# Kernel optimization log

Hardware: AMD Instinct MI355X
Metric: run time of the kernel (lower is better)

Reference implementation:

```python
import jax, jax.numpy as jnp
import numpy as np
import math

B, C, L = 64, 16, 4096
EMB, DEPTH, NEXP = 256, 2, 4
SHAPE, STRIDE = 8, 4
NPATCH = (L - SHAPE) // STRIDE + 1  # 1023
SPARSE = 0.5
NF = 32

def gelu(x):
    return jax.nn.gelu(x, approximate=False)

def conv1d(x, w, stride=1, pad=0):
    return jax.lax.conv_general_dilated(x, w, (stride,), [(pad, pad)],
                                        dimension_numbers=('NCH', 'OIH', 'NCH'))

def rmsnorm(x, g):
    # F.normalize(x, dim=-1) * gamma * sqrt(D)
    n = jnp.sqrt(jnp.sum(x * x, axis=-1, keepdims=True))
    return x / jnp.maximum(n, 1e-12) * g * (x.shape[-1] ** 0.5)

def setup_inputs():
    ks = jax.random.split(jax.random.key(0), 16)
    r = lambda i, s: jax.random.normal(ks[i], s, jnp.float32) * 0.02
    return dict(
        x=jax.random.normal(ks[0], (B, C, L), jnp.float32),
        epoch=100, warm_up=50,
        emb_w=r(1, (EMB, C, SHAPE)), emb_b=jnp.zeros((EMB,), jnp.float32),
        pos_embed=r(2, (1, NPATCH, EMB)),
        attn_w1=r(3, (EMB, 8)), attn_b1=jnp.zeros((8,), jnp.float32),
        attn_w2=r(4, (8, 1)), attn_b2=jnp.zeros((1,), jnp.float32),
        gate_w=r(5, (EMB, NEXP)), gate_b=jnp.zeros((NEXP,), jnp.float32),
        ex_w1=r(6, (NEXP, EMB, EMB)), ex_b1=jnp.zeros((NEXP, EMB), jnp.float32),
        ex_w2=r(7, (NEXP, EMB, EMB)), ex_b2=jnp.zeros((NEXP, EMB), jnp.float32),
        moe_gamma=jnp.ones((EMB,), jnp.float32),
        norm1_g=jnp.ones((DEPTH, EMB), jnp.float32),
        norm2_g=jnp.ones((DEPTH, EMB), jnp.float32),
        bott_w=r(8, (DEPTH, NF, EMB, 1)),
        conv_w39=r(9, (DEPTH, NF, NF, 39)),
        conv_w19=r(10, (DEPTH, NF, NF, 19)),
        conv_w9=r(11, (DEPTH, NF, NF, 9)),
        mp_w=r(12, (DEPTH, NF, EMB, 1)),
        bn_g=jnp.ones((DEPTH, 4 * NF), jnp.float32),
        bn_b=jnp.zeros((DEPTH, 4 * NF), jnp.float32),
        proj_w=r(13, (DEPTH, 4 * NF, EMB)),
        proj_b=jnp.zeros((DEPTH, EMB), jnp.float32),
        head_w=r(14, (EMB, 1)), head_b=jnp.zeros((1,), jnp.float32),
    )

def _forward(x, epoch, warm_up, emb_w, emb_b, pos_embed, attn_w1, attn_b1,
             attn_w2, attn_b2, gate_w, gate_b, ex_w1, ex_b1, ex_w2, ex_b2,
             moe_gamma, norm1_g, norm2_g, bott_w, conv_w39, conv_w19, conv_w9,
             mp_w, bn_g, bn_b, proj_w, proj_b, head_w, head_b):
    def attn(h):  # (B,N,D) -> (B,N,1) sigmoid importance scores
        return jax.nn.sigmoid(jnp.tanh(h @ attn_w1 + attn_b1) @ attn_w2 + attn_b2)

    def moe(h):  # top-1 routed MoE; compute all experts densely, select via one-hot
        Bm, Nm, D = h.shape
        hf = h.reshape(-1, D)  # (T, D)
        logits = jax.nn.softmax(hf @ gate_w + gate_b, axis=-1)  # (T, E)
        top_idx = jnp.argmax(logits, axis=-1)
        top_val = jnp.max(logits, axis=-1, keepdims=True)
        mid = gelu(jnp.einsum('td,edh->eth', hf, ex_w1) + ex_b1[:, None, :])
        ye = jnp.einsum('eth,ehd->etd', mid, ex_w2) + ex_b2[:, None, :]
        sel = jax.nn.one_hot(top_idx, NEXP, dtype=h.dtype)  # (T, E)
        out = jnp.einsum('etd,te->td', ye, sel)
        y = rmsnorm((hf + out * top_val).reshape(Bm, Nm, D), moe_gamma)
        imp = logits.sum(0)
        load = jnp.var(imp, ddof=1) / (imp.mean() ** 2 + 1e-10)
        return gelu(y), load

    def inception(xc, i):  # xc: (B, D, T) -> (B, 4*NF, T)
        xb = conv1d(xc, bott_w[i])  # bottleneck 1x1 -> NF channels
        mp = jax.lax.reduce_window(xc, -jnp.inf, jax.lax.max, (1, 1, 3),
                                   (1, 1, 1), [(0, 0), (0, 0), (1, 1)])
        out = jnp.concatenate([conv1d(xb, conv_w39[i], pad=19),
                               conv1d(xb, conv_w19[i], pad=9),
                               conv1d(xb, conv_w9[i], pad=4),
                               conv1d(mp, mp_w[i])], axis=1)
        # BatchNorm1d eval mode: running mean 0 / var 1, affine gamma/beta
        out = out * (bn_g[i] / np.float32(np.sqrt(1.0 + 1e-5)))[None, :, None] \
              + bn_b[i][None, :, None]
        return gelu(out)

    def incep_branch(h, i):  # (B,N,D) -> (B,N,D)
        io = inception(jnp.transpose(h, (0, 2, 1)), i)
        return jnp.transpose(io, (0, 2, 1)) @ proj_w[i] + proj_b[i]

    h = conv1d(x, emb_w, stride=STRIDE) + emb_b[None, :, None]  # (B, EMB, N)
    h = jnp.transpose(h, (0, 2, 1)) + pos_embed  # N == NPATCH -> no interp
    # pos_drop is identity at inference

    schedule = np.linspace(0.0, SPARSE, DEPTH)
    total_loss = jnp.zeros((), h.dtype)
    end_scores = None
    for i in range(DEPTH):
        ratio = 1.0 if epoch < warm_up else 1.0 - float(schedule[i])
        is_last = (i == DEPTH - 1)
        N = h.shape[1]
        x_n = rmsnorm(h, norm1_g[i])
        scores = attn(x_n)  # (B, N, 1)
        if ratio < 1.0 and N > 2:
            left_k = max(math.ceil(ratio * N), 1)
            xs = x_n * scores
            idx = jnp.sort(jax.lax.top_k(scores[..., 0], left_k)[1], axis=1)
            left_x = jnp.take_along_axis(xs, idx[:, :, None], axis=1)
            # sum of non-topk tokens == total sum minus topk sum
            extra = xs.sum(1, keepdims=True) - left_x.sum(1, keepdims=True)
            h = jnp.concatenate([left_x, extra], axis=1)  # (B, left_k+1, D)
            x_n2 = rmsnorm(h, norm2_g[i])
            moe_out, loss = moe(x_n2)
            h = h + moe_out + incep_branch(x_n2, i)
            total_loss = total_loss + loss
        else:
            h = x_n * scores
            h = h + incep_branch(rmsnorm(h, norm2_g[i]), i)
        if is_last:
            end_scores = attn(h)  # dropout identity; scores on pre-gelu x
        h = gelu(h)
    logits = h @ head_w + head_b  # (B, N', 1)
    cls = (logits * end_scores).mean(axis=1)  # (B, 1)
    return cls[..., 0], total_loss

def reference(x, epoch, warm_up, emb_w, emb_b, pos_embed, attn_w1, attn_b1,
              attn_w2, attn_b2, gate_w, gate_b, ex_w1, ex_b1, ex_w2, ex_b2,
              moe_gamma, norm1_g, norm2_g, bott_w, conv_w39, conv_w19, conv_w9,
              mp_w, bn_g, bn_b, proj_w, proj_b, head_w, head_b):
    return _forward(x, epoch, warm_up, emb_w, emb_b, pos_embed, attn_w1,
                    attn_b1, attn_w2, attn_b2, gate_w, gate_b, ex_w1, ex_b1,
                    ex_w2, ex_b2, moe_gamma, norm1_g, norm2_g, bott_w,
                    conv_w39, conv_w19, conv_w9, mp_w, bn_g, bn_b, proj_w,
                    proj_b, head_w, head_b)
```

## Files before the change

### kernel.cpp

```cpp
#include <hip/hip_runtime.h>
#include <math.h>

#define BB 64
#define EMB 256
#define N0 1023
#define N1 513
#define NTOK0 (BB * N0)
#define NTOK1 (BB * N1)
#define GCH 16

typedef __attribute__((ext_vector_type(8))) short short8;
typedef __attribute__((ext_vector_type(4))) float f32x4;

__device__ __forceinline__ float gelu_f(float x) {
    return 0.5f * x * (1.0f + erff(x * 0.7071067811865476f));
}

__device__ __forceinline__ float4 gelu4(float4 v) {
    return make_float4(gelu_f(v.x), gelu_f(v.y), gelu_f(v.z), gelu_f(v.w));
}

__device__ __forceinline__ float wave_reduce(float v) {
#pragma unroll
    for (int o = 32; o > 0; o >>= 1) v += __shfl_down(v, o, 64);
    return v;
}

__device__ __forceinline__ unsigned short f2bf(float f) {
    unsigned int u = __float_as_uint(f);
    u = (u + 0x7FFFu + ((u >> 16) & 1u)) >> 16;
    return (unsigned short)u;
}
__device__ __forceinline__ float bf2f(unsigned short h) {
    return __uint_as_float(((unsigned int)h) << 16);
}
__device__ __forceinline__ float4 bf4_to_f4(ushort4 h) {
    return make_float4(bf2f(h.x), bf2f(h.y), bf2f(h.z), bf2f(h.w));
}

__global__ void transpose_fused(const float* __restrict__ bott, float* __restrict__ bwt0,
                                float* __restrict__ bwt1,
                                const float* __restrict__ mpw, float* __restrict__ mwt0,
                                float* __restrict__ mwt1,
                                float* __restrict__ imp, int* __restrict__ counts) {
    int idx = blockIdx.x * 256 + threadIdx.x;
    if (blockIdx.x == 0 && threadIdx.x >= 252) {
        int i = threadIdx.x - 252;
        imp[i] = 0.0f; counts[i] = 0;
    }
    const float* src; float* dst; int base;
    if (idx < 8192)        { src = bott;         dst = bwt0;  base = 0; }
    else if (idx < 16384)  { src = bott + 8192;  dst = bwt1;  base = 8192; }
    else if (idx < 24576)  { src = mpw;          dst = mwt0;  base = 16384; }
    else if (idx < 32768)  { src = mpw + 8192;   dst = mwt1;  base = 24576; }
    else return;
    int local = idx - base;
    int o = local / 256, ik = local % 256;
    dst[ik * 32 + o] = src[local];
}

__global__ void convert_bf16(const float* __restrict__ ew1, const float* __restrict__ ew2,
                             const float* __restrict__ pjw,
                             const float* __restrict__ cw39, const float* __restrict__ cw19,
                             const float* __restrict__ cw9, const float* __restrict__ embw,
                             unsigned short* __restrict__ w1t, unsigned short* __restrict__ w2t,
                             unsigned short* __restrict__ pjwb,
                             unsigned short* __restrict__ cwh, unsigned short* __restrict__ cwl,
                             unsigned short* __restrict__ ewh, unsigned short* __restrict__ ewl) {
    int idx = blockIdx.x * 256 + threadIdx.x;
    if (idx < 262144) {
        int e = idx >> 16, r = idx & 65535, n = r >> 8, k = r & 255;
        w1t[idx] = f2bf(ew1[(e << 16) + (k << 8) + n]);
    } else if (idx < 524288) {
        int j = idx - 262144;
        int e = j >> 16, r = j & 65535, n = r >> 8, k = r & 255;
        w2t[j] = f2bf(ew2[(e << 16) + (k << 8) + n]);
    } else if (idx < 589824) {
        pjwb[idx - 524288] = f2bf(pjw[idx - 524288]);
    } else if (idx < 727040) {
        int j = idx - 589824;
        int d = j / 68608, r = j % 68608;
        const float* src; int KT, rr;
        if (r < 39936)      { src = cw39; KT = 39; rr = r; }
        else if (r < 59392) { src = cw19; KT = 19; rr = r - 39936; }
        else                { src = cw9;  KT = 9;  rr = r - 59392; }
        int KK = KT * 32;
        int fo = rr / KK, jj = rr % KK, k = jj >> 5, fi = jj & 31;
        float w = src[(((d * 32 + fo) * 32) + fi) * KT + k];
        unsigned short h = f2bf(w);
        cwh[j] = h;
        cwl[j] = f2bf(w - bf2f(h));
    } else if (idx < 759808) {
        int j = idx - 727040;
        float w = embw[j];
        unsigned short h = f2bf(w);
        ewh[j] = h;
        ewl[j] = f2bf(w - bf2f(h));
    }
}

__global__ __launch_bounds__(256, 2)
void embed_mfma(const float* __restrict__ x, const unsigned short* __restrict__ ewh,
                const unsigned short* __restrict__ ewl, const float* __restrict__ emb_b,
                const float* __restrict__ pos, float* __restrict__ A) {
    int b = blockIdx.y;
    int n0 = blockIdx.x * 64;
    __shared__ __align__(16) unsigned short tokh[64 * 128];
    __shared__ __align__(16) unsigned short tokl[64 * 128];
    int tid = threadIdx.x;
#pragma unroll
    for (int it = 0; it < 4; it++) {
        int idx = tid + it * 256;
        int m = idx & 63, c = idx >> 6;
        int tok = n0 + m;
        float v[8] = {0.f, 0.f, 0.f, 0.f, 0.f, 0.f, 0.f, 0.f};
        if (tok < N0) {
            const float* p = x + ((size_t)b * 16 + c) * 4096 + 4 * tok;
            float4 a = *(const float4*)p;
            float4 bq = *(const float4*)(p + 4);
            v[0] = a.x; v[1] = a.y; v[2] = a.z; v[3] = a.w;
            v[4] = bq.x; v[5] = bq.y; v[6] = bq.z; v[7] = bq.w;
        }
        short8 hv, lv;
#pragma unroll
        for (int j = 0; j < 8; j++) {
            unsigned short hh = f2bf(v[j]);
            hv[j] = (short)hh;
            lv[j] = (short)f2bf(v[j] - bf2f(hh));
        }
        int si = (m << 7) + ((c << 3) ^ ((m & 7) << 3));
        *(short8*)(&tokh[si]) = hv;
        *(short8*)(&tokl[si]) = lv;
    }
    __syncthreads();

    int lane = tid & 63, wid = tid >> 6;
    int nb = wid << 6;
    int arow = lane & 15;
    int kgrp = (lane >> 4) << 3;
    int rb = (lane >> 4) << 2;

    f32x4 acc[4][4];
#pragma unroll
    for (int mt = 0; mt < 4; mt++)
#pragma unroll
        for (int nt = 0; nt < 4; nt++) acc[mt][nt] = f32x4{0.f, 0.f, 0.f, 0.f};

    for (int ks = 0; ks < 4; ks++) {
        int kk = (ks << 5) + kgrp;
        short8 ah[4], al[4], bh[4], bl[4];
#pragma unroll
        for (int mt = 0; mt < 4; mt++) {
            int m = (mt << 4) + arow;
            int si = (m << 7) + (kk ^ ((m & 7) << 3));
            ah[mt] = *(const short8*)(&tokh[si]);
            al[mt] = *(const short8*)(&tokl[si]);
        }
#pragma unroll
        for (int nt = 0; nt < 4; nt++) {
            int n = nb + (nt << 4) + arow;
            bh[nt] = *(const short8*)(&ewh[(n << 7) + kk]);
            bl[nt] = *(const short8*)(&ewl[(n << 7) + kk]);
        }
#pragma unroll
        for (int mt = 0; mt < 4; mt++) {
#pragma unroll
            for (int nt = 0; nt < 4; nt++) {
                acc[mt][nt] = __builtin_amdgcn_mfma_f32_16x16x32_bf16(ah[mt], bh[nt], acc[mt][nt], 0, 0, 0);
                acc[mt][nt] = __builtin_amdgcn_mfma_f32_16x16x32_bf16(al[mt], bh[nt], acc[mt][nt], 0, 0, 0);
                acc[mt][nt] = __builtin_amdgcn_mfma_f32_16x16x32_bf16(ah[mt], bl[nt], acc[mt][nt], 0, 0, 0);
            }
        }
    }

    float eb[4];
#pragma unroll
    for (int nt = 0; nt < 4; nt++) eb[nt] = emb_b[nb + (nt << 4) + arow];
#pragma unroll
    for (int mt = 0; mt < 4; mt++) {
#pragma unroll
        for (int nt = 0; nt < 4; nt++) {
            int n = nb + (nt << 4) + arow;
#pragma unroll
            for (int r = 0; r < 4; r++) {
                int m = (mt << 4) + rb + r;
                int tok = n0 + m;
                if (tok < N0)
                    A[((size_t)b * N0 + tok) * 256 + n] =
                        acc[mt][nt][r] + eb[nt] + pos[(size_t)tok * 256 + n];
            }
        }
    }
}

__global__ void norm_attn_kernel(const float* __restrict__ in, float* __restrict__ outv,
                                 float* __restrict__ score_out, const float* __restrict__ g,
                                 const float* __restrict__ w1, const float* __restrict__ b1,
                                 const float* __restrict__ w2, const float* __restrict__ b2,
                                 int scale_out, int pregelu,
                                 float* __restrict__ outv2, const float* __restrict__ g2,
                                 int T) {
    int wid = threadIdx.x >> 6, lane = threadIdx.x & 63;
    int t = blockIdx.x * 4 + wid;
    if (t >= T) return;
    float4 v = ((const float4*)(in + (size_t)t * 256))[lane];
    if (pregelu) v = gelu4(v);
    float4 xn = v;
    if (g != nullptr) {
        float ss = v.x * v.x + v.y * v.y + v.z * v.z + v.w * v.w;
        ss = wave_reduce(ss);
        ss = __shfl(ss, 0, 64);
        float inv = 16.0f / fmaxf(sqrtf(ss), 1e-12f);
        float4 g4 = ((const float4*)g)[lane];
        xn.x = v.x * inv * g4.x; xn.y = v.y * inv * g4.y;
        xn.z = v.z * inv * g4.z; xn.w = v.w * inv * g4.w;
    }
    float p[8];
#pragma unroll
    for (int j = 0; j < 8; j++) p[j] = 0.0f;
    const float xv[4] = {xn.x, xn.y, xn.z, xn.w};
#pragma unroll
    for (int c = 0; c < 4; c++) {
        const float4* wr = (const float4*)(w1 + (4 * lane + c) * 8);
        float4 wa = wr[0], wb = wr[1];
        float xx = xv[c];
        p[0] += xx * wa.x; p[1] += xx * wa.y; p[2] += xx * wa.z; p[3] += xx * wa.w;
        p[4] += xx * wb.x; p[5] += xx * wb.y; p[6] += xx * wb.z; p[7] += xx * wb.w;
    }
#pragma unroll
    for (int j = 0; j < 8; j++) p[j] = wave_reduce(p[j]);
    float sc = 0.0f;
    if (lane == 0) {
        float z = b2[0];
#pragma unroll
        for (int j = 0; j < 8; j++) z += tanhf(p[j] + b1[j]) * w2[j];
        sc = 1.0f / (1.0f + expf(-z));
        if (score_out) score_out[t] = sc;
    }
    sc = __shfl(sc, 0, 64);
    if (outv) {
        float m = scale_out ? sc : 1.0f;
        float4 o = make_float4(xn.x * m, xn.y * m, xn.z * m, xn.w * m);
        ((float4*)(outv + (size_t)t * 256))[lane] = o;
    }
    if (outv2) {
        float ss2 = xn.x * xn.x + xn.y * xn.y + xn.z * xn.z + xn.w * xn.w;
        ss2 = wave_reduce(ss2);
        ss2 = __shfl(ss2, 0, 64);
        float inv2 = 16.0f / fmaxf(sqrtf(ss2), 1e-12f);
        float4 q4 = ((const float4*)g2)[lane];
        float4 o;
        o.x = xn.x * inv2 * q4.x; o.y = xn.y * inv2 * q4.y;
        o.z = xn.z * inv2 * q4.z; o.w = xn.w * inv2 * q4.w;
        ((float4*)(outv2 + (size_t)t * 256))[lane] = o;
    }
}

__global__ void rmsnorm_kernel(const float* __restrict__ in, float* __restrict__ out,
                               const float* __restrict__ g, int T) {
    int wid = threadIdx.x >> 6, lane = threadIdx.x & 63;
    int t = blockIdx.x * 4 + wid;
    if (t >= T) return;
    float4 v = ((const float4*)(in + (size_t)t * 256))[lane];
    float ss = v.x * v.x + v.y * v.y + v.z * v.z + v.w * v.w;
    ss = wave_reduce(ss);
    ss = __shfl(ss, 0, 64);
    float inv = 16.0f / fmaxf(sqrtf(ss), 1e-12f);
    float4 g4 = ((const float4*)g)[lane];
    float4 o;
    o.x = v.x * inv * g4.x; o.y = v.y * inv * g4.y;
    o.z = v.z * inv * g4.z; o.w = v.w * inv * g4.w;
    ((float4*)(out + (size_t)t * 256))[lane] = o;
}

__global__ void pw_kernel(const float* __restrict__ xn, const float* __restrict__ bwt,
                          const float* __restrict__ mwt, const float* __restrict__ bng,
                          const float* __restrict__ bnb, float* __restrict__ xb,
                          float* __restrict__ cat, int N) {
    int b = blockIdx.y;
    int t0 = blockIdx.x * 16;
    const float* xbase = xn + (size_t)b * N * 256;
    __shared__ float xt[18][256];
    __shared__ float xm[16][256];
    for (int idx = threadIdx.x; idx < 18 * 256; idx += 256) {
        int r = idx >> 8, d = idx & 255;
        int t = t0 + r - 1;
        xt[r][d] = (t >= 0 && t < N) ? xbase[(size_t)t * 256 + d] : -INFINITY;
    }
    __syncthreads();
    for (int idx = threadIdx.x; idx < 16 * 256; idx += 256) {
        int r = idx >> 8, d = idx & 255;
        xm[r][d] = fmaxf(fmaxf(xt[r][d], xt[r + 1][d]), xt[r + 2][d]);
    }
    __syncthreads();
    int f = threadIdx.x & 31;
    int gI = threadIdx.x >> 5;
    float accb[2] = {0.0f, 0.0f}, accm[2] = {0.0f, 0.0f};
    for (int d0 = 0; d0 < 256; d0++) {
        float wb = bwt[d0 * 32 + f];
        float wm = mwt[d0 * 32 + f];
#pragma unroll
        for (int i = 0; i < 2; i++) {
            int tt = gI * 2 + i;
            accb[i] += xt[1 + tt][d0] * wb;
            accm[i] += xm[tt][d0] * wm;
        }
    }
    const float BN_DIV = 1.0000050f;
    float scl = bng[96 + f] / BN_DIV;
    float sh = bnb[96 + f];
    for (int i = 0; i < 2; i++) {
        int t = t0 + gI * 2 + i;
        if (t < N) {
            xb[((size_t)b * N + t) * 32 + f] = accb[i];
            cat[((size_t)b * N + t) * 128 + 96 + f] = gelu_f(accm[i] * scl + sh);
        }
    }
}

__global__ __launch_bounds__(256, 4)
void conv_mfma(const float* __restrict__ xb, const unsigned short* __restrict__ wh,
               const unsigned short* __restrict__ wl, const float* __restrict__ bng,
               const float* __restrict__ bnb, float* __restrict__ cat, int N) {
    int b = blockIdx.y;
    int t0 = blockIdx.x * 64;
    __shared__ __align__(16) unsigned short tokh[104 * 40];
    __shared__ __align__(16) unsigned short tokl[104 * 40];
    const float* xbase = xb + (size_t)b * N * 32;
    int tid = threadIdx.x;
    for (int idx = tid; idx < 104 * 16; idx += 256) {
        int r = idx >> 4, p = (idx & 15) << 1;
        int t = t0 - 19 + r;
        float vx = 0.f, vy = 0.f;
        if (t >= 0 && t < N) {
            const float2 v = *(const float2*)(xbase + (size_t)t * 32 + p);
            vx = v.x; vy = v.y;
        }
        unsigned short h0 = f2bf(vx), h1 = f2bf(vy);
        unsigned short l0 = f2bf(vx - bf2f(h0)), l1 = f2bf(vy - bf2f(h1));
        *(unsigned int*)(&tokh[r * 40 + p]) = (unsigned)h0 | ((unsigned)h1 << 16);
        *(unsigned int*)(&tokl[r * 40 + p]) = (unsigned)l0 | ((unsigned)l1 << 16);
    }
    __syncthreads();
    int lane = tid & 63, wid = tid >> 6;
    int arow = lane & 15, kgrp = (lane >> 4) << 3;
    int rb = (lane >> 4) << 2;
    f32x4 acc[3][2];
#pragma unroll
    for (int i = 0; i < 3; i++) {
        acc[i][0] = f32x4{0.f, 0.f, 0.f, 0.f};
        acc[i][1] = f32x4{0.f, 0.f, 0.f, 0.f};
    }

#define CONV_BR(KT, BOFF, WOFF, BR)                                                        \
    {                                                                                      \
        const int KK = (KT) * 32;                                                          \
        int r0 = (WOFF) + wid * 16 + arow;                                                 \
        const unsigned short* whp = wh + (BOFF) + arow * KK + kgrp;                        \
        const unsigned short* wlp = wl + (BOFF) + arow * KK + kgrp;                        \
        for (int k = 0; k < (KT); k++) {                                                   \
            short8 ah = *(const short8*)(&tokh[(r0 + k) * 40 + kgrp]);                     \
            short8 al = *(const short8*)(&tokl[(r0 + k) * 40 + kgrp]);                     \
            short8 bh0 = *(const short8*)(&whp[k * 32]);                                   \
            short8 bl0 = *(const short8*)(&wlp[k * 32]);                                   \
            short8 bh1 = *(const short8*)(&whp[16 * KK + k * 32]);                         \
            short8 bl1 = *(const short8*)(&wlp[16 * KK + k * 32]);                         \
            acc[BR][0] = __builtin_amdgcn_mfma_f32_16x16x32_bf16(ah, bh0, acc[BR][0], 0, 0, 0); \
            acc[BR][1] = __builtin_amdgcn_mfma_f32_16x16x32_bf16(ah, bh1, acc[BR][1], 0, 0, 0); \
            acc[BR][0] = __builtin_amdgcn_mfma_f32_16x16x32_bf16(al, bh0, acc[BR][0], 0, 0, 0); \
            acc[BR][1] = __builtin_amdgcn_mfma_f32_16x16x32_bf16(al, bh1, acc[BR][1], 0, 0, 0); \
            acc[BR][0] = __builtin_amdgcn_mfma_f32_16x16x32_bf16(ah, bl0, acc[BR][0], 0, 0, 0); \
            acc[BR][1] = __builtin_amdgcn_mfma_f32_16x16x32_bf16(ah, bl1, acc[BR][1], 0, 0, 0); \
        }                                                                                  \
    }

    CONV_BR(39, 0, 0, 0)
    CONV_BR(19, 39936, 10, 1)
    CONV_BR(9, 59392, 15, 2)
#undef CONV_BR

    const float BN_DIV = 1.0000050f;
    const int COFFS[3] = {0, 32, 64};
#pragma unroll
    for (int br = 0; br < 3; br++) {
#pragma unroll
        for (int nt = 0; nt < 2; nt++) {
            int fo = COFFS[br] + nt * 16 + arow;
            float scl = bng[fo] / BN_DIV;
            float sh = bnb[fo];
#pragma unroll
            for (int r = 0; r < 4; r++) {
                int t = t0 + wid * 16 + rb + r;
                if (t < N)
                    cat[((size_t)b * N + t) * 128 + fo] = gelu_f(acc[br][nt][r] * scl + sh);
            }
        }
    }
}

__global__ void proj_kernel(const float* __restrict__ cat, const unsigned short* __restrict__ pw,
                            const float* __restrict__ pb, float* __restrict__ A, int TN) {
    int t0 = blockIdx.x * 16;
    __shared__ float cl[16][128];
    for (int v = threadIdx.x; v < 16 * 32; v += 256) {
        int r = v >> 5, c4 = v & 31;
        int t = t0 + r;
        ((float4*)cl[r])[c4] = (t < TN) ? ((const float4*)(cat + (size_t)t * 128))[c4]
                                        : make_float4(0.f, 0.f, 0.f, 0.f);
    }
    __syncthreads();
    int c0 = threadIdx.x & 63;
    int g = threadIdx.x >> 6;
    float acc[4][4];
#pragma unroll
    for (int i = 0; i < 4; i++)
#pragma unroll
        for (int j = 0; j < 4; j++) acc[i][j] = 0.0f;
    for (int f = 0; f < 128; f++) {
        float4 w = bf4_to_f4(((const ushort4*)(pw + (size_t)f * 256))[c0]);
        float v0 = cl[g * 4 + 0][f], v1 = cl[g * 4 + 1][f];
        float v2 = cl[g * 4 + 2][f], v3 = cl[g * 4 + 3][f];
        acc[0][0] += v0 * w.x; acc[0][1] += v0 * w.y; acc[0][2] += v0 * w.z; acc[0][3] += v0 * w.w;
        acc[1][0] += v1 * w.x; acc[1][1] += v1 * w.y; acc[1][2] += v1 * w.z; acc[1][3] += v1 * w.w;
        acc[2][0] += v2 * w.x; acc[2][1] += v2 * w.y; acc[2][2] += v2 * w.z; acc[2][3] += v2 * w.w;
        acc[3][0] += v3 * w.x; acc[3][1] += v3 * w.y; acc[3][2] += v3 * w.z; acc[3][3] += v3 * w.w;
    }
    float4 bias = ((const float4*)pb)[c0];
#pragma unroll
    for (int i = 0; i < 4; i++) {
        int t = t0 + g * 4 + i;
        if (t < TN) {
            float4* ap = (float4*)(A + (size_t)t * 256) + c0;
            float4 a = *ap;
            a.x += acc[i][0] + bias.x; a.y += acc[i][1] + bias.y;
            a.z += acc[i][2] + bias.z; a.w += acc[i][3] + bias.w;
            *ap = a;
        }
    }
}

__global__ __launch_bounds__(1024) void topk_kernel(const float* __restrict__ s,
                                                    int* __restrict__ selpos) {
    int b = blockIdx.x;
    int tid = threadIdx.x;
    __shared__ float srt[1024];
    __shared__ int buf[1024];
    __shared__ int Gtot_s;
    float val = (tid < N0) ? s[(size_t)b * N0 + tid] : -INFINITY;
    srt[tid] = val;
    __syncthreads();
    for (int ksz = 2; ksz <= 1024; ksz <<= 1) {
        for (int j = ksz >> 1; j > 0; j >>= 1) {
            int ixj = tid ^ j;
            if (ixj > tid) {
                float a = srt[tid], c = srt[ixj];
                bool up = ((tid & ksz) == 0);
                if ((a > c) == up) { srt[tid] = c; srt[ixj] = a; }
            }
            __syncthreads();
        }
    }
    float thr = srt[512];
    __syncthreads();
    int isG = (val > thr) ? 1 : 0;
    int isE = (val == thr) ? 1 : 0;
    buf[tid] = isG;
    __syncthreads();
    for (int off = 1; off < 1024; off <<= 1) {
        int cur = buf[tid];
        int add = (tid >= off) ? buf[tid - off] : 0;
        __syncthreads();
        buf[tid] = cur + add;
        __syncthreads();
    }
    if (tid == 0) Gtot_s = buf[1023];
    __syncthreads();
    int Gtot = Gtot_s;
    int Eneed = 512 - Gtot;
    buf[tid] = isE;
    __syncthreads();
    for (int off = 1; off < 1024; off <<= 1) {
        int cur = buf[tid];
        int add = (tid >= off) ? buf[tid - off] : 0;
        __syncthreads();
        buf[tid] = cur + add;
        __syncthreads();
    }
    int eqExcl = buf[tid] - isE;
    int sel = (isG || (isE && eqExcl < Eneed)) ? 1 : 0;
    __syncthreads();
    buf[tid] = sel;
    __syncthreads();
    for (int off = 1; off < 1024; off <<= 1) {
        int cur = buf[tid];
        int add = (tid >= off) ? buf[tid - off] : 0;
        __syncthreads();
        buf[tid] = cur + add;
        __syncthreads();
    }
    int pos = buf[tid] - sel;
    selpos[b * 1024 + tid] = sel ? pos : -1;
}

__global__ void scatter_kernel(const float* __restrict__ xn, const float* __restrict__ s,
                               const int* __restrict__ selpos, float* __restrict__ A,
                               float* __restrict__ part) {
    int b = blockIdx.y;
    int chunk = blockIdx.x;
    int wid = threadIdx.x >> 6, lane = threadIdx.x & 63;
    int t0 = chunk * 64;
    __shared__ float sl[64];
    __shared__ int pl[64];
    if (threadIdx.x < 64) {
        int t = t0 + threadIdx.x;
        sl[threadIdx.x] = (t < N0) ? s[(size_t)b * N0 + t] : 0.0f;
        pl[threadIdx.x] = (t < N0) ? selpos[b * 1024 + t] : -1;
    }
    __syncthreads();
    const float* xbase = xn + ((size_t)b * N0 + t0) * 256;
    float* obase = A + (size_t)b * N1 * 256;
    float4 nonsel = make_float4(0.f, 0.f, 0.f, 0.f);
    int tmax = (t0 + 64 <= N0) ? 64 : (N0 - t0);
    for (int i = wid; i < tmax; i += 4) {
        float sc = sl[i];
        float4 v = ((const float4*)(xbase + (size_t)i * 256))[lane];
        v.x *= sc; v.y *= sc; v.z *= sc; v.w *= sc;
        int p = pl[i];
        if (p >= 0) ((float4*)(obase + (size_t)p * 256))[lane] = v;
        else { nonsel.x += v.x; nonsel.y += v.y; nonsel.z += v.z; nonsel.w += v.w; }
    }
    ((float4*)(part + ((size_t)(b * GCH + chunk) * 4 + wid) * 256))[lane] = nonsel;
}

__global__ void extra_kernel(const float* __restrict__ part, float* __restrict__ A) {
    int b = blockIdx.x, d = threadIdx.x;
    float acc = 0.0f;
    for (int c = 0; c < GCH * 4; c++) acc += part[((size_t)b * GCH * 4 + c) * 256 + d];
    A[((size_t)b * N1 + 512) * 256 + d] = acc;
}

__global__ void gate_kernel(const float* __restrict__ xn2, const float* __restrict__ gw,
                            const float* __restrict__ gb, float* __restrict__ topval,
                            int* __restrict__ buckets, int* __restrict__ counts,
                            float* __restrict__ imp, int T) {
    int tid = threadIdx.x;
    int t = blockIdx.x * 256 + tid;
    __shared__ float4 gws[256];
    __shared__ int lcount[4];
    __shared__ int lbase[4];
    __shared__ float limp[4];
    gws[tid] = ((const float4*)gw)[tid];
    if (tid < 4) { lcount[tid] = 0; limp[tid] = 0.0f; }
    __syncthreads();
    bool valid = (t < T);
    float a0 = 0, a1 = 0, a2 = 0, a3 = 0;
    if (valid) {
        const float4* xb4 = (const float4*)(xn2 + (size_t)t * 256);
#pragma unroll 8
        for (int d4 = 0; d4 < 64; d4++) {
            float4 xv = xb4[d4];
            float4 w0 = gws[4 * d4], w1 = gws[4 * d4 + 1];
            float4 w2 = gws[4 * d4 + 2], w3 = gws[4 * d4 + 3];
            a0 += xv.x * w0.x + xv.y * w1.x + xv.z * w2.x + xv.w * w3.x;
            a1 += xv.x * w0.y + xv.y * w1.y + xv.z * w2.y + xv.w * w3.y;
            a2 += xv.x * w0.z + xv.y * w1.z + xv.z * w2.z + xv.w * w3.z;
            a3 += xv.x * w0.w + xv.y * w1.w + xv.z * w2.w + xv.w * w3.w;
        }
    }
    float q0 = 0, q1 = 0, q2 = 0, q3 = 0;
    int eid = 0;
    int lrank = 0;
    if (valid) {
        float l0 = a0 + gb[0], l1 = a1 + gb[1], l2 = a2 + gb[2], l3 = a3 + gb[3];
        float m = fmaxf(fmaxf(l0, l1), fmaxf(l2, l3));
        float e0 = expf(l0 - m), e1 = expf(l1 - m), e2 = expf(l2 - m), e3 = expf(l3 - m);
        float ssum = e0 + e1 + e2 + e3;
        q0 = e0 / ssum; q1 = e1 / ssum; q2 = e2 / ssum; q3 = e3 / ssum;
        float bv = q0;
        if (q1 > bv) { bv = q1; eid = 1; }
        if (q2 > bv) { bv = q2; eid = 2; }
        if (q3 > bv) { bv = q3; eid = 3; }
        topval[t] = bv;
        lrank = atomicAdd(&lcount[eid], 1);
    }
    float r0 = wave_reduce(q0), r1 = wave_reduce(q1);
    float r2 = wave_reduce(q2), r3 = wave_reduce(q3);
    if ((tid & 63) == 0) {
        atomicAdd(&limp[0], r0); atomicAdd(&limp[1], r1);
        atomicAdd(&limp[2], r2); atomicAdd(&limp[3], r3);
    }
    __syncthreads();
    if (tid < 4) {
        lbase[tid] = atomicAdd(&counts[tid], lcount[tid]);
        atomicAdd(&imp[tid], limp[tid]);
    }
    __syncthreads();
    if (valid) buckets[eid * T + lbase[eid] + lrank] = t;
}

#define FFN_KLOOP(WPTR)                                                                    \
    for (int ks = 0; ks < 8; ks++) {                                                       \
        int kk = (ks << 5) + kgrp;                                                         \
        short8 ah[4], al[4], bw[4];                                                        \
        _Pragma("unroll")                                                                  \
        for (int mt = 0; mt < 4; mt++) {                                                   \
            int m = (mt << 4) + arow;                                                      \
            int si = (m << 8) + (kk ^ ((m & 7) << 3));                                     \
            ah[mt] = *(const short8*)(&tokh[si]);                                          \
            al[mt] = *(const short8*)(&tokl[si]);                                          \
        }                                                                                  \
        _Pragma("unroll")                                                                  \
        for (int nt = 0; nt < 4; nt++)                                                     \
            bw[nt] = *(const short8*)(&WPTR[((size_t)(nb + (nt << 4) + arow) << 8) + kk]); \
        _Pragma("unroll")                                                                  \
        for (int mt = 0; mt < 4; mt++) {                                                   \
            _Pragma("unroll")                                                              \
            for (int nt = 0; nt < 4; nt++) {                                               \
                acc[mt][nt] = __builtin_amdgcn_mfma_f32_16x16x32_bf16(                     \
                    ah[mt], bw[nt], acc[mt][nt], 0, 0, 0);                                 \
                acc[mt][nt] = __builtin_amdgcn_mfma_f32_16x16x32_bf16(                     \
                    al[mt], bw[nt], acc[mt][nt], 0, 0, 0);                                 \
            }                                                                              \
        }                                                                                  \
    }

__global__ __launch_bounds__(256, 2)
void ffn_kernel(const float* __restrict__ xn2, const unsigned short* __restrict__ w1t,
                const float* __restrict__ b1, const unsigned short* __restrict__ w2t,
                const float* __restrict__ b2, const float* __restrict__ topval,
                const int* __restrict__ buckets, const int* __restrict__ counts,
                float* __restrict__ C, int T) {
    int e = blockIdx.y;
    int cnt = counts[e];
    int base = blockIdx.x * 64;
    if (base >= cnt) return;
    __shared__ __align__(16) unsigned short tokh[64 * 256];
    __shared__ __align__(16) unsigned short tokl[64 * 256];
    __shared__ int tids[64];
    __shared__ float tv[64];
    int tid = threadIdx.x;
    if (tid < 64) {
        int idx = base + tid;
        int t = (idx < cnt) ? buckets[e * T + idx] : -1;
        tids[tid] = t;
        tv[tid] = (t >= 0) ? topval[t] : 0.0f;
    }
    __syncthreads();
#pragma unroll
    for (int it = 0; it < 8; it++) {
        int cc = tid + it * 256;
        int m = cc >> 5, d0 = (cc & 31) << 3;
        int t = tids[m];
        float4 a = make_float4(0.f, 0.f, 0.f, 0.f), b = a;
        if (t >= 0) {
            const float4* p = (const float4*)(xn2 + (size_t)t * 256 + d0);
            a = p[0]; b = p[1];
        }
        float v[8] = {a.x, a.y, a.z, a.w, b.x, b.y, b.z, b.w};
        short8 hv, lv;
#pragma unroll
        for (int j = 0; j < 8; j++) {
            unsigned short hh = f2bf(v[j]);
            hv[j] = (short)hh;
            lv[j] = (short)f2bf(v[j] - bf2f(hh));
        }
        int si = (m << 8) + (d0 ^ ((m & 7) << 3));
        *(short8*)(&tokh[si]) = hv;
        *(short8*)(&tokl[si]) = lv;
    }
    __syncthreads();

    int lane = tid & 63, wid = tid >> 6;
    int nb = wid << 6;
    int arow = lane & 15;
    int kgrp = (lane >> 4) << 3;
    int rb = (lane >> 4) << 2;
    const unsigned short* W1 = w1t + ((size_t)e << 16);
    const unsigned short* W2 = w2t + ((size_t)e << 16);

    f32x4 acc[4][4];
#pragma unroll
    for (int mt = 0; mt < 4; mt++)
#pragma unroll
        for (int nt = 0; nt < 4; nt++) acc[mt][nt] = f32x4{0.f, 0.f, 0.f, 0.f};

    FFN_KLOOP(W1)

    float b1v[4];
#pragma unroll
    for (int nt = 0; nt < 4; nt++) b1v[nt] = b1[(e << 8) + nb + (nt << 4) + arow];
    __syncthreads();
#pragma unroll
    for (int mt = 0; mt < 4; mt++) {
#pragma unroll
        for (int nt = 0; nt < 4; nt++) {
            int kd = nb + (nt << 4) + arow;
#pragma unroll
            for (int r = 0; r < 4; r++) {
                int m = (mt << 4) + rb + r;
                float mid = gelu_f(acc[mt][nt][r] + b1v[nt]);
                unsigned short hh = f2bf(mid);
                int si = (m << 8) + (kd ^ ((m & 7) << 3));
                tokh[si] = hh;
                tokl[si] = f2bf(mid - bf2f(hh));
            }
        }
    }
    __syncthreads();

#pragma unroll
    for (int mt = 0; mt < 4; mt++)
#pragma unroll
        for (int nt = 0; nt < 4; nt++) acc[mt][nt] = f32x4{0.f, 0.f, 0.f, 0.f};

    FFN_KLOOP(W2)

    float b2v[4];
#pragma unroll
    for (int nt = 0; nt < 4; nt++) b2v[nt] = b2[(e << 8) + nb + (nt << 4) + arow];
#pragma unroll
    for (int mt = 0; mt < 4; mt++) {
        int tt[4]; float tvv[4];
#pragma unroll
        for (int r = 0; r < 4; r++) {
            int m = (mt << 4) + rb + r;
            tt[r] = tids[m];
            tvv[r] = tv[m];
        }
#pragma unroll
        for (int nt = 0; nt < 4; nt++) {
            int n = nb + (nt << 4) + arow;
#pragma unroll
            for (int r = 0; r < 4; r++) {
                int t = tt[r];
                if (t >= 0) {
                    float val = acc[mt][nt][r] + b2v[nt];
                    C[(size_t)t * 256 + n] =
                        xn2[(size_t)t * 256 + n] + val * tvv[r];
                }
            }
        }
    }
}

__global__ void moe_add_kernel(const float* __restrict__ C, float* __restrict__ A,
                               const float* __restrict__ gamma, int T) {
    int wid = threadIdx.x >> 6, lane = threadIdx.x & 63;
    int t = blockIdx.x * 4 + wid;
    if (t >= T) return;
    float4 v = ((const float4*)(C + (size_t)t * 256))[lane];
    float ss = v.x * v.x + v.y * v.y + v.z * v.z + v.w * v.w;
    ss = wave_reduce(ss);
    ss = __shfl(ss, 0, 64);
    float inv = 16.0f / fmaxf(sqrtf(ss), 1e-12f);
    float4 g4 = ((const float4*)gamma)[lane];
    float4* ap = (float4*)(A + (size_t)t * 256) + lane;
    float4 a = *ap;
    a.x += gelu_f(v.x * inv * g4.x); a.y += gelu_f(v.y * inv * g4.y);
    a.z += gelu_f(v.z * inv * g4.z); a.w += gelu_f(v.w * inv * g4.w);
    *ap = a;
}

__global__ void endhead_kernel(const float* __restrict__ A, const float* __restrict__ w1,
                               const float* __restrict__ b1, const float* __restrict__ w2,
                               const float* __restrict__ b2, const float* __restrict__ hw,
                               const float* __restrict__ hb, float* __restrict__ contrib,
                               int T) {
    int wid = threadIdx.x >> 6, lane = threadIdx.x & 63;
    int t = blockIdx.x * 4 + wid;
    if (t >= T) return;
    float4 v = ((const float4*)(A + (size_t)t * 256))[lane];
    float p[8];
#pragma unroll
    for (int j = 0; j < 8; j++) p[j] = 0.0f;
    const float xv[4] = {v.x, v.y, v.z, v.w};
#pragma unroll
    for (int c = 0; c < 4; c++) {
        const float4* wr = (const float4*)(w1 + (4 * lane + c) * 8);
        float4 wa = wr[0], wb = wr[1];
        float xx = xv[c];
        p[0] += xx * wa.x; p[1] += xx * wa.y; p[2] += xx * wa.z; p[3] += xx * wa.w;
        p[4] += xx * wb.x; p[5] += xx * wb.y; p[6] += xx * wb.z; p[7] += xx * wb.w;
    }
    float4 h4 = ((const float4*)hw)[lane];
    float hp = gelu_f(v.x) * h4.x + gelu_f(v.y) * h4.y + gelu_f(v.z) * h4.z + gelu_f(v.w) * h4.w;
#pragma unroll
    for (int j = 0; j < 8; j++) p[j] = wave_reduce(p[j]);
    hp = wave_reduce(hp);
    if (lane == 0) {
        float z = b2[0];
#pragma unroll
        for (int j = 0; j < 8; j++) z += tanhf(p[j] + b1[j]) * w2[j];
        float sc = 1.0f / (1.0f + expf(-z));
        contrib[t] = (hp + hb[0]) * sc * (1.0f / (float)N1);
    }
}

__global__ void finalsum_kernel(const float* __restrict__ contrib,
                                const float* __restrict__ imp, float* __restrict__ out) {
    int b = blockIdx.x, tid = threadIdx.x;
    __shared__ float red[4];
    const float* cb = contrib + (size_t)b * N1;
    float v = cb[tid] + cb[256 + tid];
    if (tid == 0) v += cb[512];
    float s = wave_reduce(v);
    int wid = tid >> 6, lane = tid & 63;
    if (lane == 0) red[wid] = s;
    __syncthreads();
    if (tid == 0) {
        out[b] = red[0] + red[1] + red[2] + red[3];
        if (b == 0) {
            float i0 = imp[0], i1 = imp[1], i2 = imp[2], i3 = imp[3];
            float mean = (i0 + i1 + i2 + i3) * 0.25f;
            float var = ((i0 - mean) * (i0 - mean) + (i1 - mean) * (i1 - mean) +
                         (i2 - mean) * (i2 - mean) + (i3 - mean) * (i3 - mean)) / 3.0f;
            out[64] = var / (mean * mean + 1e-10f);
        }
    }
}

extern "C" void kernel_launch(void* const* d_in, const int* in_sizes, int n_in,
                              void* d_out, int out_size, void* d_ws, size_t ws_size,
                              hipStream_t stream) {
    const float* x    = (const float*)d_in[0];
    const float* embw = (const float*)d_in[3];
    const float* embb = (const float*)d_in[4];
    const float* pos  = (const float*)d_in[5];
    const float* aw1  = (const float*)d_in[6];
    const float* ab1  = (const float*)d_in[7];
    const float* aw2  = (const float*)d_in[8];
    const float* ab2  = (const float*)d_in[9];
    const float* gw   = (const float*)d_in[10];
    const float* gb   = (const float*)d_in[11];
    const float* ew1  = (const float*)d_in[12];
    const float* eb1  = (const float*)d_in[13];
    const float* ew2  = (const float*)d_in[14];
    const float* eb2  = (const float*)d_in[15];
    const float* mg   = (const float*)d_in[16];
    const float* n1g  = (const float*)d_in[17];
    const float* n2g  = (const float*)d_in[18];
    const float* bott = (const float*)d_in[19];
    const float* cw39 = (const float*)d_in[20];
    const float* cw19 = (const float*)d_in[21];
    const float* cw9  = (const float*)d_in[22];
    const float* mpw  = (const float*)d_in[23];
    const float* bng  = (const float*)d_in[24];
    const float* bnb  = (const float*)d_in[25];
    const float* pjw  = (const float*)d_in[26];
    const float* pjb  = (const float*)d_in[27];
    const float* hw   = (const float*)d_in[28];
    const float* hb   = (const float*)d_in[29];
    float* out = (float*)d_out;

    float* W = (float*)d_ws;
    size_t off = 0;
    auto alloc = [&](size_t n) { float* p = W + off; off += n; return p; };
    float* A    = alloc((size_t)NTOK0 * 256);
    float* Bb   = alloc((size_t)NTOK0 * 256);
    float* CD   = alloc((size_t)NTOK1 * 256);
    float* XB   = alloc((size_t)NTOK0 * 32);
    float* sS   = alloc(NTOK0);
    float* ctb  = alloc(NTOK1);
    float* tval = alloc(NTOK1);
    float* imp  = alloc(4);
    float* part = alloc((size_t)BB * GCH * 4 * 256);
    float* bwt0 = alloc(256 * 32);  float* bwt1 = alloc(256 * 32);
    float* mwt0 = alloc(256 * 32);  float* mwt1 = alloc(256 * 32);
    off = (off + 3) & ~(size_t)3;
    unsigned short* w1t  = (unsigned short*)(W + off); off += 262144 / 2;
    unsigned short* w2t  = (unsigned short*)(W + off); off += 262144 / 2;
    unsigned short* pjwb = (unsigned short*)(W + off); off += 65536 / 2;
    unsigned short* cwh  = (unsigned short*)(W + off); off += 137216 / 2;
    unsigned short* cwl  = (unsigned short*)(W + off); off += 137216 / 2;
    unsigned short* ewh  = (unsigned short*)(W + off); off += 32768 / 2;
    unsigned short* ewl  = (unsigned short*)(W + off); off += 32768 / 2;
    int* selpos  = (int*)(W + off); off += (size_t)BB * 1024;
    int* buckets = (int*)(W + off); off += (size_t)4 * NTOK1;
    int* counts  = (int*)(W + off); off += 4;

    transpose_fused<<<128, 256, 0, stream>>>(bott, bwt0, bwt1, mpw, mwt0, mwt1, imp, counts);
    convert_bf16<<<2968, 256, 0, stream>>>(ew1, ew2, pjw, cw39, cw19, cw9, embw,
                                           w1t, w2t, pjwb, cwh, cwl, ewh, ewl);

    embed_mfma<<<dim3(16, BB), 256, 0, stream>>>(x, ewh, ewl, embb, pos, A);
    norm_attn_kernel<<<NTOK0 / 4, 256, 0, stream>>>(A, A, nullptr, n1g, aw1, ab1, aw2, ab2,
                                                    1, 0, Bb, n2g, NTOK0);
    pw_kernel<<<dim3(64, BB), 256, 0, stream>>>(Bb, bwt0, mwt0, bng, bnb, XB, CD, N0);
    conv_mfma<<<dim3(16, BB), 256, 0, stream>>>(XB, cwh, cwl, bng, bnb, CD, N0);
    proj_kernel<<<(NTOK0 + 15) / 16, 256, 0, stream>>>(CD, pjwb, pjb, A, NTOK0);

    norm_attn_kernel<<<NTOK0 / 4, 256, 0, stream>>>(A, Bb, sS, n1g + 256, aw1, ab1, aw2, ab2,
                                                    0, 1, nullptr, nullptr, NTOK0);
    topk_kernel<<<BB, 1024, 0, stream>>>(sS, selpos);
    scatter_kernel<<<dim3(GCH, BB), 256, 0, stream>>>(Bb, sS, selpos, A, part);
    extra_kernel<<<BB, 256, 0, stream>>>(part, A);
    rmsnorm_kernel<<<NTOK1 / 4, 256, 0, stream>>>(A, Bb, n2g + 256, NTOK1);
    gate_kernel<<<(NTOK1 + 255) / 256, 256, 0, stream>>>(Bb, gw, gb, tval, buckets, counts, imp,
                                                         NTOK1);
    ffn_kernel<<<dim3((NTOK1 + 63) / 64, 4), 256, 0, stream>>>(Bb, w1t, eb1, w2t, eb2, tval,
                                                               buckets, counts, CD, NTOK1);
    moe_add_kernel<<<NTOK1 / 4, 256, 0, stream>>>(CD, A, mg, NTOK1);
    pw_kernel<<<dim3((N1 + 15) / 16, BB), 256, 0, stream>>>(Bb, bwt1, mwt1, bng + 128, bnb + 128,
                                                            XB, CD, N1);
    conv_mfma<<<dim3(9, BB), 256, 0, stream>>>(XB, cwh + 68608, cwl + 68608,
                                               bng + 128, bnb + 128, CD, N1);
    proj_kernel<<<(NTOK1 + 15) / 16, 256, 0, stream>>>(CD, pjwb + 32768, pjb + 256, A, NTOK1);
    endhead_kernel<<<NTOK1 / 4, 256, 0, stream>>>(A, aw1, ab1, aw2, ab2, hw, hb, ctb, NTOK1);
    finalsum_kernel<<<BB, 256, 0, stream>>>(ctb, imp, out);
}
```

Before: 906.1 us.

## Run inception pointwise bottleneck and maxpool convs on bf16x3 MFMA

Replaces the scalar FP32 pointwise bottleneck and maxpool-projection kernel with an MFMA version. Activations are split into bf16 hi/lo pairs in swizzled shared memory, and three bf16 MFMAs per step approximate FP32 accuracy. Tokens per block go from 16 to 32. The weight transpose kernel is folded into the bf16 conversion kernel, which now also produces hi/lo bottleneck and maxpool weights and zeroes the counters, saving one launch. Risks include small precision loss from the 3-term split and the -inf padding encoded as bf16 0xFF80.

```diff
diff --git a/kernel.cpp b/kernel.cpp
--- a/kernel.cpp
+++ b/kernel.cpp
@@ -38,36 +38,23 @@
     return make_float4(bf2f(h.x), bf2f(h.y), bf2f(h.z), bf2f(h.w));
 }
 
-__global__ void transpose_fused(const float* __restrict__ bott, float* __restrict__ bwt0,
-                                float* __restrict__ bwt1,
-                                const float* __restrict__ mpw, float* __restrict__ mwt0,
-                                float* __restrict__ mwt1,
-                                float* __restrict__ imp, int* __restrict__ counts) {
+__global__ void convert_bf16(const float* __restrict__ ew1, const float* __restrict__ ew2,
+                             const float* __restrict__ pjw,
+                             const float* __restrict__ cw39, const float* __restrict__ cw19,
+                             const float* __restrict__ cw9, const float* __restrict__ embw,
+                             const float* __restrict__ bott, const float* __restrict__ mpw,
+                             unsigned short* __restrict__ w1t, unsigned short* __restrict__ w2t,
+                             unsigned short* __restrict__ pjwb,
+                             unsigned short* __restrict__ cwh, unsigned short* __restrict__ cwl,
+                             unsigned short* __restrict__ ewh, unsigned short* __restrict__ ewl,
+                             unsigned short* __restrict__ bth, unsigned short* __restrict__ btl,
+                             unsigned short* __restrict__ mph, unsigned short* __restrict__ mpl,
+                             float* __restrict__ imp, int* __restrict__ counts) {
     int idx = blockIdx.x * 256 + threadIdx.x;
     if (blockIdx.x == 0 && threadIdx.x >= 252) {
         int i = threadIdx.x - 252;
         imp[i] = 0.0f; counts[i] = 0;
     }
-    const float* src; float* dst; int base;
-    if (idx < 8192)        { src = bott;         dst = bwt0;  base = 0; }
-    else if (idx < 16384)  { src = bott + 8192;  dst = bwt1;  base = 8192; }
-    else if (idx < 24576)  { src = mpw;          dst = mwt0;  base = 16384; }
-    else if (idx < 32768)  { src = mpw + 8192;   dst = mwt1;  base = 24576; }
-    else return;
-    int local = idx - base;
-    int o = local / 256, ik = local % 256;
-    dst[ik * 32 + o] = src[local];
-}
-
-__global__ void convert_bf16(const float* __restrict__ ew1, const float* __restrict__ ew2,
-                             const float* __restrict__ pjw,
-                             const float* __restrict__ cw39, const float* __restrict__ cw19,
-                             const float* __restrict__ cw9, const float* __restrict__ embw,
-                             unsigned short* __restrict__ w1t, unsigned short* __restrict__ w2t,
-                             unsigned short* __restrict__ pjwb,
-                             unsigned short* __restrict__ cwh, unsigned short* __restrict__ cwl,
-                             unsigned short* __restrict__ ewh, unsigned short* __restrict__ ewl) {
-    int idx = blockIdx.x * 256 + threadIdx.x;
     if (idx < 262144) {
         int e = idx >> 16, r = idx & 65535, n = r >> 8, k = r & 255;
         w1t[idx] = f2bf(ew1[(e << 16) + (k << 8) + n]);
@@ -96,6 +83,18 @@
         unsigned short h = f2bf(w);
         ewh[j] = h;
         ewl[j] = f2bf(w - bf2f(h));
+    } else if (idx < 776192) {
+        int j = idx - 759808;
+        float w = bott[j];
+        unsigned short h = f2bf(w);
+        bth[j] = h;
+        btl[j] = f2bf(w - bf2f(h));
+    } else if (idx < 792576) {
+        int j = idx - 776192;
+        float w = mpw[j];
+        unsigned short h = f2bf(w);
+        mph[j] = h;
+        mpl[j] = f2bf(w - bf2f(h));
     }
 }
 
@@ -273,47 +272,120 @@
     ((float4*)(out + (size_t)t * 256))[lane] = o;
 }
 
-__global__ void pw_kernel(const float* __restrict__ xn, const float* __restrict__ bwt,
-                          const float* __restrict__ mwt, const float* __restrict__ bng,
-                          const float* __restrict__ bnb, float* __restrict__ xb,
-                          float* __restrict__ cat, int N) {
+__global__ __launch_bounds__(256, 2)
+void pw_mfma(const float* __restrict__ xn, const unsigned short* __restrict__ bwh,
+             const unsigned short* __restrict__ bwl, const unsigned short* __restrict__ mwh,
+             const unsigned short* __restrict__ mwl, const float* __restrict__ bng,
+             const float* __restrict__ bnb, float* __restrict__ xb,
+             float* __restrict__ cat, int N) {
     int b = blockIdx.y;
-    int t0 = blockIdx.x * 16;
+    int t0 = blockIdx.x * 32;
+    __shared__ __align__(16) unsigned short xth[34 * 256];
+    __shared__ __align__(16) unsigned short xtl[34 * 256];
+    __shared__ __align__(16) unsigned short xmh[32 * 256];
+    __shared__ __align__(16) unsigned short xml[32 * 256];
     const float* xbase = xn + (size_t)b * N * 256;
-    __shared__ float xt[18][256];
-    __shared__ float xm[16][256];
-    for (int idx = threadIdx.x; idx < 18 * 256; idx += 256) {
-        int r = idx >> 8, d = idx & 255;
-        int t = t0 + r - 1;
-        xt[r][d] = (t >= 0 && t < N) ? xbase[(size_t)t * 256 + d] : -INFINITY;
-    }
-    __syncthreads();
-    for (int idx = threadIdx.x; idx < 16 * 256; idx += 256) {
-        int r = idx >> 8, d = idx & 255;
-        xm[r][d] = fmaxf(fmaxf(xt[r][d], xt[r + 1][d]), xt[r + 2][d]);
-    }
-    __syncthreads();
-    int f = threadIdx.x & 31;
-    int gI = threadIdx.x >> 5;
-    float accb[2] = {0.0f, 0.0f}, accm[2] = {0.0f, 0.0f};
-    for (int d0 = 0; d0 < 256; d0++) {
-        float wb = bwt[d0 * 32 + f];
-        float wm = mwt[d0 * 32 + f];
-#pragma unroll
-        for (int i = 0; i < 2; i++) {
-            int tt = gI * 2 + i;
-            accb[i] += xt[1 + tt][d0] * wb;
-            accm[i] += xm[tt][d0] * wm;
-        }
-    }
+    int tid = threadIdx.x;
+    for (int idx = tid; idx < 34 * 32; idx += 256) {
+        int r = idx >> 5, p = (idx & 31) << 3;
+        int t = t0 - 1 + r;
+        short8 hv, lv;
+        if (t >= 0 && t < N) {
+            const float4* q = (const float4*)(xbase + (size_t)t * 256 + p);
+            float4 a = q[0], c = q[1];
+            float v[8] = {a.x, a.y, a.z, a.w, c.x, c.y, c.z, c.w};
+#pragma unroll
+            for (int j = 0; j < 8; j++) {
+                unsigned short hh = f2bf(v[j]);
+                hv[j] = (short)hh;
+                lv[j] = (short)f2bf(v[j] - bf2f(hh));
+            }
+        } else {
+#pragma unroll
+            for (int j = 0; j < 8; j++) { hv[j] = (short)0xFF80; lv[j] = 0; }
+        }
+        int si = (r << 8) + (p ^ ((r & 7) << 3));
+        *(short8*)(&xth[si]) = hv;
+        *(short8*)(&xtl[si]) = lv;
+    }
+    __syncthreads();
+    for (int idx = tid; idx < 32 * 32; idx += 256) {
+        int r = idx >> 5, p = (idx & 31) << 3;
+        int s0 = ((r + 0) << 8) + (p ^ (((r + 0) & 7) << 3));
+        int s1 = ((r + 1) << 8) + (p ^ (((r + 1) & 7) << 3));
+        int s2 = ((r + 2) << 8) + (p ^ (((r + 2) & 7) << 3));
+        short8 h0 = *(const short8*)(&xth[s0]), l0 = *(const short8*)(&xtl[s0]);
+        short8 h1 = *(const short8*)(&xth[s1]), l1 = *(const short8*)(&xtl[s1]);
+        short8 h2 = *(const short8*)(&xth[s2]), l2 = *(const short8*)(&xtl[s2]);
+        short8 hv, lv;
+#pragma unroll
+        for (int j = 0; j < 8; j++) {
+            float a = bf2f((unsigned short)h0[j]) + bf2f((unsigned short)l0[j]);
+            float c = bf2f((unsigned short)h1[j]) + bf2f((unsigned short)l1[j]);
+            float d = bf2f((unsigned short)h2[j]) + bf2f((unsigned short)l2[j]);
+            float m = fmaxf(fmaxf(a, c), d);
+            unsigned short hh = f2bf(m);
+            hv[j] = (short)hh;
+            lv[j] = (short)f2bf(m - bf2f(hh));
+        }
+        int si = (r << 8) + (p ^ ((r & 7) << 3));
+        *(short8*)(&xmh[si]) = hv;
+        *(short8*)(&xml[si]) = lv;
+    }
+    __syncthreads();
+
+    int lane = tid & 63, wid = tid >> 6;
+    int mt = wid & 1, path = wid >> 1;
+    int arow = lane & 15, kgrp = (lane >> 4) << 3, rb = (lane >> 4) << 2;
+    const unsigned short* Wh = path ? mwh : bwh;
+    const unsigned short* Wl = path ? mwl : bwl;
+    f32x4 acc[2];
+    acc[0] = f32x4{0.f, 0.f, 0.f, 0.f};
+    acc[1] = f32x4{0.f, 0.f, 0.f, 0.f};
+
+    int m = (mt << 4) + arow;
+    int rowA = path ? m : (m + 1);
+    const unsigned short* Ah = path ? xmh : xth;
+    const unsigned short* Al = path ? xml : xtl;
+    for (int ks = 0; ks < 8; ks++) {
+        int kk = (ks << 5) + kgrp;
+        int si = (rowA << 8) + (kk ^ ((rowA & 7) << 3));
+        short8 ah = *(const short8*)(&Ah[si]);
+        short8 al = *(const short8*)(&Al[si]);
+#pragma unroll
+        for (int nt = 0; nt < 2; nt++) {
+            int n = (nt << 4) + arow;
+            short8 bh = *(const short8*)(&Wh[n * 256 + kk]);
+            short8 bl = *(const short8*)(&Wl[n * 256 + kk]);
+            acc[nt] = __builtin_amdgcn_mfma_f32_16x16x32_bf16(ah, bh, acc[nt], 0, 0, 0);
+            acc[nt] = __builtin_amdgcn_mfma_f32_16x16x32_bf16(al, bh, acc[nt], 0, 0, 0);
+            acc[nt] = __builtin_amdgcn_mfma_f32_16x16x32_bf16(ah, bl, acc[nt], 0, 0, 0);
+        }
+    }
+
     const float BN_DIV = 1.0000050f;
-    float scl = bng[96 + f] / BN_DIV;
-    float sh = bnb[96 + f];
-    for (int i = 0; i < 2; i++) {
-        int t = t0 + gI * 2 + i;
-        if (t < N) {
-            xb[((size_t)b * N + t) * 32 + f] = accb[i];
-            cat[((size_t)b * N + t) * 128 + 96 + f] = gelu_f(accm[i] * scl + sh);
+    if (path == 0) {
+#pragma unroll
+        for (int nt = 0; nt < 2; nt++) {
+            int n = (nt << 4) + arow;
+#pragma unroll
+            for (int r = 0; r < 4; r++) {
+                int t = t0 + (mt << 4) + rb + r;
+                if (t < N) xb[((size_t)b * N + t) * 32 + n] = acc[nt][r];
+            }
+        }
+    } else {
+#pragma unroll
+        for (int nt = 0; nt < 2; nt++) {
+            int n = (nt << 4) + arow;
+            float scl = bng[96 + n] / BN_DIV;
+            float sh = bnb[96 + n];
+#pragma unroll
+            for (int r = 0; r < 4; r++) {
+                int t = t0 + (mt << 4) + rb + r;
+                if (t < N)
+                    cat[((size_t)b * N + t) * 128 + 96 + n] = gelu_f(acc[nt][r] * scl + sh);
+            }
         }
     }
 }
@@ -864,8 +936,6 @@
     float* tval = alloc(NTOK1);
     float* imp  = alloc(4);
     float* part = alloc((size_t)BB * GCH * 4 * 256);
-    float* bwt0 = alloc(256 * 32);  float* bwt1 = alloc(256 * 32);
-    float* mwt0 = alloc(256 * 32);  float* mwt1 = alloc(256 * 32);
     off = (off + 3) & ~(size_t)3;
     unsigned short* w1t  = (unsigned short*)(W + off); off += 262144 / 2;
     unsigned short* w2t  = (unsigned short*)(W + off); off += 262144 / 2;
@@ -874,18 +944,22 @@
     unsigned short* cwl  = (unsigned short*)(W + off); off += 137216 / 2;
     unsigned short* ewh  = (unsigned short*)(W + off); off += 32768 / 2;
     unsigned short* ewl  = (unsigned short*)(W + off); off += 32768 / 2;
+    unsigned short* bth  = (unsigned short*)(W + off); off += 16384 / 2;
+    unsigned short* btl  = (unsigned short*)(W + off); off += 16384 / 2;
+    unsigned short* mph  = (unsigned short*)(W + off); off += 16384 / 2;
+    unsigned short* mpl  = (unsigned short*)(W + off); off += 16384 / 2;
     int* selpos  = (int*)(W + off); off += (size_t)BB * 1024;
     int* buckets = (int*)(W + off); off += (size_t)4 * NTOK1;
     int* counts  = (int*)(W + off); off += 4;
 
-    transpose_fused<<<128, 256, 0, stream>>>(bott, bwt0, bwt1, mpw, mwt0, mwt1, imp, counts);
-    convert_bf16<<<2968, 256, 0, stream>>>(ew1, ew2, pjw, cw39, cw19, cw9, embw,
-                                           w1t, w2t, pjwb, cwh, cwl, ewh, ewl);
+    convert_bf16<<<3096, 256, 0, stream>>>(ew1, ew2, pjw, cw39, cw19, cw9, embw, bott, mpw,
+                                           w1t, w2t, pjwb, cwh, cwl, ewh, ewl,
+                                           bth, btl, mph, mpl, imp, counts);
 
     embed_mfma<<<dim3(16, BB), 256, 0, stream>>>(x, ewh, ewl, embb, pos, A);
     norm_attn_kernel<<<NTOK0 / 4, 256, 0, stream>>>(A, A, nullptr, n1g, aw1, ab1, aw2, ab2,
                                                     1, 0, Bb, n2g, NTOK0);
-    pw_kernel<<<dim3(64, BB), 256, 0, stream>>>(Bb, bwt0, mwt0, bng, bnb, XB, CD, N0);
+    pw_mfma<<<dim3(32, BB), 256, 0, stream>>>(Bb, bth, btl, mph, mpl, bng, bnb, XB, CD, N0);
     conv_mfma<<<dim3(16, BB), 256, 0, stream>>>(XB, cwh, cwl, bng, bnb, CD, N0);
     proj_kernel<<<(NTOK0 + 15) / 16, 256, 0, stream>>>(CD, pjwb, pjb, A, NTOK0);
 
@@ -900,8 +974,9 @@
     ffn_kernel<<<dim3((NTOK1 + 63) / 64, 4), 256, 0, stream>>>(Bb, w1t, eb1, w2t, eb2, tval,
                                                                buckets, counts, CD, NTOK1);
     moe_add_kernel<<<NTOK1 / 4, 256, 0, stream>>>(CD, A, mg, NTOK1);
-    pw_kernel<<<dim3((N1 + 15) / 16, BB), 256, 0, stream>>>(Bb, bwt1, mwt1, bng + 128, bnb + 128,
-                                                            XB, CD, N1);
+    pw_mfma<<<dim3((N1 + 31) / 32, BB), 256, 0, stream>>>(Bb, bth + 8192, btl + 8192,
+                                                          mph + 8192, mpl + 8192,
+                                                          bng + 128, bnb + 128, XB, CD, N1);
     conv_mfma<<<dim3(9, BB), 256, 0, stream>>>(XB, cwh + 68608, cwl + 68608,
                                                bng + 128, bnb + 128, CD, N1);
     proj_kernel<<<(NTOK1 + 15) / 16, 256, 0, stream>>>(CD, pjwb + 32768, pjb + 256, A, NTOK1);
```

New measurement: 842.1 us. 7.1% less time.
